# Performance work log

Hardware: AMD Instinct MI355X
Metric: run time of the kernel (lower is better)

## Reference

```python
import jax, jax.numpy as jnp
import numpy as np

B, T, NF, C, H, TOPK = 4, 8, 8192, 384, 12, 32
D = C // H
SCALE = D ** -0.5  # qk_scale=None -> head_dim**-0.5


def setup_inputs() -> dict:
    key = jax.random.key(0)
    ks = jax.random.split(key, 4)
    x = jax.random.normal(ks[0], (B, T + NF, C), jnp.float32)
    qs_w = jax.random.normal(ks[1], (T, C, C), jnp.float32) * (C ** -0.5)
    kv_w = jax.random.normal(ks[2], (C, 2 * C), jnp.float32) * (C ** -0.5)
    experts_w = jax.random.normal(ks[3], (T, C, C), jnp.float32) * (C ** -0.5)
    return {"x": x, "qs_w": qs_w, "kv_w": kv_w, "experts_w": experts_w}


def reference(x, qs_w, kv_w, experts_w):
    # x: [B, T+NF, C]; first T tokens are task tokens, rest are feature tokens
    feature = x[:, T:, :]                                          # [B,NF,C]
    kv = (feature @ kv_w).reshape(B, NF, 2, H, D)                  # out dim splits [2,H,D]
    k = kv[:, :, 0].transpose(0, 2, 1, 3)                          # [B,H,NF,D]
    v = kv[:, :, 1].transpose(0, 2, 1, 3)                          # [B,H,NF,D]
    # per-task query linears (no bias), one task token each
    q = jnp.einsum('btc,tco->bto', x[:, :T, :], qs_w)              # [B,T,C]
    q = q.reshape(B, T, H, D).transpose(0, 2, 1, 3)                # [B,H,T,D]
    attn = jnp.einsum('bhtd,bhnd->bhtn', q, k) * SCALE             # [B,H,T,NF]
    vals, idx = jax.lax.top_k(attn, TOPK)                          # [B,H,T,K]
    w = jax.nn.softmax(vals, axis=-1)                              # softmax over top-k only
    # attn_token = (scatter(topk softmax) @ v) == weighted gather of v rows
    v_g = jnp.take_along_axis(v[:, :, None], idx[..., None], axis=3)   # [B,H,T,K,D]
    attn_token = jnp.einsum('bhtk,bhtkd->bhtd', w, v_g)
    attn_token = attn_token.transpose(0, 2, 1, 3).reshape(B, T, C)     # [B,T,C]
    # gather raw feature tokens at top-k indices, weight, scatter into padded zeros
    fm = feature.reshape(B, NF, H, D).transpose(0, 2, 1, 3)        # [B,H,NF,D]
    f_g = jnp.take_along_axis(fm[:, :, None], idx[..., None], axis=3) * w[..., None]  # [B,H,T,K,D]
    bi = jnp.arange(B)[:, None, None, None]
    hi = jnp.arange(H)[None, :, None, None]
    ti = jnp.arange(T)[None, None, :, None]
    # topk indices are unique per row -> set is well-defined
    feature_pad = jnp.zeros((B, H, T, NF, D), x.dtype).at[bi, hi, ti, idx].set(f_g)
    feature_pad = feature_pad.transpose(0, 2, 3, 1, 4).reshape(B, T, NF, C)  # [B,T,NF,C]
    # per-task expert linears; einsum with ones weight == sum over tasks
    feature_out = jnp.einsum('btnc,tco->bno', feature_pad, experts_w)  # [B,NF,C]
    token_out = jnp.einsum('btc,tco->bto', attn_token, experts_w)      # [B,T,C]
    return jnp.concatenate([token_out, feature_out], axis=1)          # [B,T+NF,C]
```

## Files before the change

kernel.cpp:

```cpp
#include <hip/hip_runtime.h>
#include <hip/hip_bf16.h>
#include <math.h>

#define B 4
#define T 8
#define NF 8192
#define C 384
#define H 12
#define TOPK 32
#define D 32
#define STOT (T + NF)
#define R (H * T)
#define KSEL 48
#define NCH 4
#define CHSZ (NF / NCH)
#define SCALE 0.17677669529663687f

typedef unsigned int uint;
typedef unsigned short ushort;
typedef short bf16x8 __attribute__((ext_vector_type(8)));
typedef float f32x4 __attribute__((ext_vector_type(4)));

__device__ __forceinline__ ushort bf16u(float a) {
  return __builtin_bit_cast(ushort, __float2bfloat16(a));
}

__device__ __forceinline__ ushort f32_key(float s) {
  uint kb = bf16u(s);
  kb ^= (kb & 0x8000u) ? 0xFFFFu : 0x8000u;
  return (ushort)kb;
}

__global__ __launch_bounds__(256) void ta_qproj_kernel(
    const float* __restrict__ x, const float* __restrict__ qs_w,
    float* __restrict__ q_part) {
  int t = blockIdx.x;
  int o0 = blockIdx.y * 64;
  int z = blockIdx.z;
  int tid = threadIdx.x;
  int o = tid & 63, ks = tid >> 6;
  __shared__ float xs[B][192];
  __shared__ float part[4][B][64];
  if (tid < 192) {
    int b = tid / 48, j4 = (tid % 48) * 4;
    *reinterpret_cast<float4*>(&xs[b][j4]) =
        *reinterpret_cast<const float4*>(x + ((size_t)b * STOT + t) * C + z * 192 + j4);
  }
  __syncthreads();
  float a0 = 0.f, a1 = 0.f, a2 = 0.f, a3 = 0.f;
  const float* w = qs_w + (size_t)t * C * C + (size_t)(z * 192 + ks * 48) * C + o0 + o;
#pragma unroll 8
  for (int c = 0; c < 48; ++c) {
    float wv = w[(size_t)c * C];
    int cj = ks * 48 + c;
    a0 += xs[0][cj] * wv;
    a1 += xs[1][cj] * wv;
    a2 += xs[2][cj] * wv;
    a3 += xs[3][cj] * wv;
  }
  part[ks][0][o] = a0; part[ks][1][o] = a1;
  part[ks][2][o] = a2; part[ks][3][o] = a3;
  __syncthreads();
  {
    int b = tid >> 6, oo = tid & 63;
    float s = part[0][b][oo] + part[1][b][oo] + part[2][b][oo] + part[3][b][oo];
    q_part[(((size_t)z * B + b) * T + t) * C + o0 + oo] = s;
  }
}

__global__ __launch_bounds__(384) void ta_fold_kernel(
    const float* __restrict__ q_part, const float* __restrict__ kv_w,
    float* __restrict__ qk_f32, ushort* __restrict__ qk_bf) {
  int b = blockIdx.x / H, h = blockIdx.x % H;
  int tid = threadIdx.x;
  __shared__ float kS[C][33];
  __shared__ float qh[T][D];
  if (tid < T * D) {
    int t = tid >> 5, d = tid & 31;
    qh[t][d] = q_part[((size_t)b * T + t) * C + h * D + d] +
               q_part[(((size_t)B + b) * T + t) * C + h * D + d];
  }
  for (int j = tid; j < C * 8; j += 384) {
    int c = j >> 3, d4 = (j & 7) * 4;
    float4 v = *reinterpret_cast<const float4*>(
        kv_w + (size_t)c * (2 * C) + h * D + d4);
    kS[c][d4 + 0] = v.x; kS[c][d4 + 1] = v.y;
    kS[c][d4 + 2] = v.z; kS[c][d4 + 3] = v.w;
  }
  __syncthreads();
  float acc[T] = {0.f, 0.f, 0.f, 0.f, 0.f, 0.f, 0.f, 0.f};
#pragma unroll
  for (int d = 0; d < D; ++d) {
    float kv = kS[tid][d];
#pragma unroll
    for (int t = 0; t < T; ++t) acc[t] += qh[t][d] * kv;
  }
#pragma unroll
  for (int t = 0; t < T; ++t) {
    size_t off = ((size_t)b * R + (size_t)h * T + t) * C + tid;
    float a = acc[t];
    qk_f32[off] = a;
    qk_bf[off] = bf16u(a);
  }
}

__global__ __launch_bounds__(256) void ta_scores_kernel(
    const float* __restrict__ x, const ushort* __restrict__ qk_bf,
    ushort* __restrict__ keys, float4* __restrict__ out4) {
  int b = blockIdx.y;
  int n0 = blockIdx.x * 64;
  int tid = threadIdx.x;
  int lane = tid & 63, w = tid >> 6;
  int row16 = lane & 15, kg = lane >> 4;
  __shared__ ushort fS[64][72];
  __shared__ ushort qS[96][72];
  f32x4 acc[6];
#pragma unroll
  for (int i = 0; i < 6; ++i) acc[i] = (f32x4){0.f, 0.f, 0.f, 0.f};

  {
    const int SL = (B * STOT * C / 4) / 512;
    int zbid = blockIdx.y * gridDim.x + blockIdx.x;
    float4 z = {0.f, 0.f, 0.f, 0.f};
    float4* dst = out4 + (size_t)zbid * SL;
    for (int j = tid; j < SL; j += 256) dst[j] = z;
  }

  const float* xb = x + ((size_t)b * STOT + T + n0) * C;
  const ushort* qb = qk_bf + (size_t)b * R * C;

  int frow = tid >> 2, fcg = (tid & 3) * 8;

#pragma unroll 1
  for (int c0 = 0; c0 < C; c0 += 32) {
    {
      const float* src = xb + (size_t)frow * C + c0 + fcg;
      float4 v0 = *reinterpret_cast<const float4*>(src);
      float4 v1 = *reinterpret_cast<const float4*>(src + 4);
      uint4 p;
      p.x = (uint)bf16u(v0.x) | ((uint)bf16u(v0.y) << 16);
      p.y = (uint)bf16u(v0.z) | ((uint)bf16u(v0.w) << 16);
      p.z = (uint)bf16u(v1.x) | ((uint)bf16u(v1.y) << 16);
      p.w = (uint)bf16u(v1.z) | ((uint)bf16u(v1.w) << 16);
      *reinterpret_cast<uint4*>(&fS[frow][fcg]) = p;
    }
#pragma unroll
    for (int s = 0; s < 2; ++s) {
      int u = tid + 256 * s;
      if (u < 384) {
        int row = u >> 2, cg = (u & 3) * 8;
        uint4 v = *reinterpret_cast<const uint4*>(qb + (size_t)row * C + c0 + cg);
        *reinterpret_cast<uint4*>(&qS[row][cg]) = v;
      }
    }
    __syncthreads();
    bf16x8 bfr = *reinterpret_cast<const bf16x8*>(&fS[w * 16 + row16][kg * 8]);
#pragma unroll
    for (int i = 0; i < 6; ++i) {
      bf16x8 afr = *reinterpret_cast<const bf16x8*>(&qS[i * 16 + row16][kg * 8]);
      acc[i] = __builtin_amdgcn_mfma_f32_16x16x32_bf16(afr, bfr, acc[i], 0, 0, 0);
    }
    __syncthreads();
  }
  int n = n0 + w * 16 + row16;
#pragma unroll
  for (int i = 0; i < 6; ++i) {
    int rbase = i * 16 + kg * 4;
#pragma unroll
    for (int reg = 0; reg < 4; ++reg) {
      keys[((size_t)b * R + rbase + reg) * NF + n] = f32_key(acc[i][reg] * SCALE);
    }
  }
}

__global__ __launch_bounds__(256) void ta_selchunk_kernel(
    const ushort* __restrict__ keys, uint* __restrict__ cand_buf) {
  int ch = blockIdx.x, rr = blockIdx.y;
  int tid = threadIdx.x;
  int lane = tid & 63, wvi = tid >> 6;
  __shared__ uint hist[4096];
  __shared__ uint cand[CHSZ];
  __shared__ uint wtot[4];
  __shared__ uint sh_piv, cnt;
  const ushort* kp = keys + (size_t)rr * NF + (size_t)ch * CHSZ;

  {
    uint4 z4 = {0u, 0u, 0u, 0u};
    uint4* hz = reinterpret_cast<uint4*>(hist);
    for (int i = tid; i < 1024; i += 256) hz[i] = z4;
  }
  if (tid == 0) cnt = 0;
  __syncthreads();
  for (int i = tid; i < CHSZ; i += 256) atomicAdd(&hist[kp[i] >> 4], 1u);
  __syncthreads();

  uint pp = 0;
#pragma unroll
  for (int j = 0; j < 16; ++j) pp += hist[tid * 16 + j];
  uint suf = pp;
#pragma unroll
  for (int off = 1; off < 64; off <<= 1) {
    uint o = __shfl_down(suf, off);
    if (lane + off < 64) suf += o;
  }
  if (lane == 0) wtot[wvi] = suf;
  __syncthreads();
  {
    uint later = 0;
    for (int wq = wvi + 1; wq < 4; ++wq) later += wtot[wq];
    uint geg = later + suf;
    uint gng = geg - pp;
    if (geg >= (uint)KSEL && gng < (uint)KSEL) {
      uint run = gng;
      int pv = 0;
      for (int j = 15; j >= 0; --j) {
        uint c = hist[tid * 16 + j];
        uint nrun = run + c;
        if (nrun >= (uint)KSEL && run < (uint)KSEL) pv = tid * 16 + j;
        run = nrun;
      }
      sh_piv = (uint)pv;
    }
  }
  __syncthreads();
  uint piv = sh_piv;
  for (int i = tid; i < CHSZ; i += 256) {
    uint u = kp[i];
    if ((u >> 4) >= piv) {
      uint s = atomicAdd(&cnt, 1u);
      cand[s] = (u << 13) | (8191u - (uint)(ch * CHSZ + i));
    }
  }
  __syncthreads();
  uint m = cnt;
  for (int i2 = tid; i2 < (int)m; i2 += 256) {
    uint me = cand[i2];
    int r = 0;
    for (uint e = 0; e < m; ++e) r += (cand[e] > me);
    if (r < KSEL) cand_buf[((size_t)rr * NCH + ch) * KSEL + r] = me;
  }
}

__global__ __launch_bounds__(384) void ta_mergetail_kernel(
    const uint* __restrict__ cand_buf, const float* __restrict__ x,
    const float* __restrict__ qk_f32, const float* __restrict__ kv_w,
    const float* __restrict__ ew, float* __restrict__ out) {
  constexpr int M = NCH * KSEL;
  int rr = blockIdx.x;
  int t = rr % T, h = (rr / T) % H, b = rr / R;
  int hD = h * D;
  int tid = threadIdx.x;
  __shared__ uint candS[M];
  __shared__ int il[KSEL];
  __shared__ float sv[KSEL];
  __shared__ int rkS[KSEL];
  __shared__ float qS[C];
  __shared__ float wl[TOPK];
  __shared__ int top_il[TOPK];
  __shared__ float fbarS[C];
  __shared__ float gS[TOPK][D];
  __shared__ float part[8][D];
  __shared__ __align__(16) float attS[D];
  __shared__ float smax, esum;

  if (tid < M) candS[tid] = cand_buf[(size_t)rr * M + tid];
  qS[tid] = qk_f32[(size_t)rr * C + tid];
  __syncthreads();
  if (tid < M) {
    uint me = candS[tid];
    int r = 0;
#pragma unroll 8
    for (int e = 0; e < M; ++e) r += (candS[e] > me);
    if (r < KSEL) il[r] = 8191 - (int)(me & 8191u);
  }
  __syncthreads();

  {
    int k = tid >> 3, j = tid & 7;
    const float* fp = x + ((size_t)b * STOT + T + il[k]) * C + j;
    float s = 0.f;
#pragma unroll 8
    for (int m2 = 0; m2 < 48; ++m2) s += fp[m2 * 8] * qS[j + m2 * 8];
    s += __shfl_down(s, 4);
    s += __shfl_down(s, 2);
    s += __shfl_down(s, 1);
    if (j == 0) sv[k] = s * SCALE;
  }
  __syncthreads();
  if (tid < KSEL) {
    float mys = sv[tid];
    int myn = il[tid];
    int r = 0;
#pragma unroll
    for (int e = 0; e < KSEL; ++e) {
      float se = sv[e];
      r += (se > mys) || (se == mys && il[e] < myn);
    }
    rkS[tid] = r;
    if (r == 0) smax = mys;
  }
  __syncthreads();
  {
    float e = 0.f;
    if (tid < KSEL && rkS[tid] < TOPK) e = expf(sv[tid] - smax);
    if (tid < 64) {
      float t2 = e;
#pragma unroll
      for (int off = 32; off; off >>= 1) t2 += __shfl_down(t2, off);
      if (tid == 0) esum = t2;
    }
    __syncthreads();
    if (tid < KSEL && rkS[tid] < TOPK) {
      wl[rkS[tid]] = e / esum;
      top_il[rkS[tid]] = il[tid];
    }
  }
  __syncthreads();

  {
    float fbar = 0.f;
    bool ing = (tid >= hD) && (tid < hD + D);
#pragma unroll 4
    for (int k = 0; k < TOPK; ++k) {
      float v = x[((size_t)b * STOT + T + top_il[k]) * C + tid];
      float wv = wl[k] * v;
      fbar += wv;
      if (ing) gS[k][tid - hD] = wv;
    }
    fbarS[tid] = fbar;
  }
  __syncthreads();

  if (tid < 256) {
    int d = tid & 31, seg = tid >> 5;
    const float* vw = kv_w + C + hD + d;
    float a0 = 0.f, a1 = 0.f;
    int cb = seg * 48;
#pragma unroll 8
    for (int c = 0; c < 48; c += 2) {
      a0 += fbarS[cb + c] * vw[(size_t)(cb + c) * (2 * C)];
      a1 += fbarS[cb + c + 1] * vw[(size_t)(cb + c + 1) * (2 * C)];
    }
    part[seg][d] = a0 + a1;
  }
  __syncthreads();
  if (tid < D) {
    float a = 0.f;
#pragma unroll
    for (int s = 0; s < 8; ++s) a += part[s][tid];
    attS[tid] = a;
  }
  __syncthreads();

  float ewc[D];
  const float* ewt = ew + (size_t)t * C * C + (size_t)hD * C + tid;
#pragma unroll
  for (int dd = 0; dd < D; ++dd) ewc[dd] = ewt[(size_t)dd * C];
  size_t obase = (size_t)b * STOT * C + tid;
#pragma unroll 1
  for (int kk = 0; kk < TOPK; ++kk) {
    float y = 0.f;
#pragma unroll
    for (int d4 = 0; d4 < D; d4 += 4) {
      float4 g4 = *reinterpret_cast<const float4*>(&gS[kk][d4]);
      y += g4.x * ewc[d4] + g4.y * ewc[d4 + 1] +
           g4.z * ewc[d4 + 2] + g4.w * ewc[d4 + 3];
    }
    atomicAdd(&out[obase + (size_t)(T + top_il[kk]) * C], y);
  }
  {
    float y = 0.f;
#pragma unroll
    for (int d4 = 0; d4 < D; d4 += 4) {
      float4 a4 = *reinterpret_cast<const float4*>(attS + d4);
      y += a4.x * ewc[d4] + a4.y * ewc[d4 + 1] +
           a4.z * ewc[d4 + 2] + a4.w * ewc[d4 + 3];
    }
    atomicAdd(&out[obase + (size_t)t * C], y);
  }
}

extern "C" void kernel_launch(void* const* d_in, const int* in_sizes, int n_in,
                              void* d_out, int out_size, void* d_ws, size_t ws_size,
                              hipStream_t stream) {
  const float* x = (const float*)d_in[0];
  const float* qs_w = (const float*)d_in[1];
  const float* kv_w = (const float*)d_in[2];
  const float* ew = (const float*)d_in[3];
  float* out = (float*)d_out;

  char* p = (char*)d_ws;
  float* qk_f32 = (float*)p;  p += (size_t)B * R * C * 4;
  ushort* qk_bf = (ushort*)p; p += (size_t)B * R * C * 2;
  ushort* keys = (ushort*)p;  p += (size_t)B * R * NF * 2;
  uint* cand_buf = (uint*)p;  p += (size_t)B * R * NCH * KSEL * 4;
  float* q_part = (float*)p;

  dim3 gq(T, C / 64, 2);
  ta_qproj_kernel<<<gq, 256, 0, stream>>>(x, qs_w, q_part);
  ta_fold_kernel<<<B * H, 384, 0, stream>>>(q_part, kv_w, qk_f32, qk_bf);
  dim3 g2(NF / 64, B);
  ta_scores_kernel<<<g2, 256, 0, stream>>>(x, qk_bf, keys, (float4*)out);
  dim3 gs(NCH, B * R);
  ta_selchunk_kernel<<<gs, 256, 0, stream>>>(keys, cand_buf);
  ta_mergetail_kernel<<<B * R, 384, 0, stream>>>(cand_buf, x, qk_f32, kv_w, ew, out);
}
```

Baseline: 83.81 us.

## Use split-bf16 triple MFMA for scores and drop fp32 rescoring of candidates

The score GEMM now splits both operands into hi and lo bf16 parts and runs three MFMAs per step, giving near-fp32 scores. It writes those scores to a full fp32 buffer, so the merge kernel ranks candidates by a lookup instead of recomputing 48 dot products from x and qk_f32. Zeroing of the output moves from the scores kernel to the selection kernel. The cost is three times the MFMA work, doubled LDS staging, and an extra 1.5 MB fp32 score write.

```diff
diff --git a/kernel.cpp b/kernel.cpp
--- a/kernel.cpp
+++ b/kernel.cpp
@@ -24,7 +24,10 @@
 __device__ __forceinline__ ushort bf16u(float a) {
   return __builtin_bit_cast(ushort, __float2bfloat16(a));
 }
-
+__device__ __forceinline__ float bf16f(ushort u) {
+  uint v = (uint)u << 16;
+  return __builtin_bit_cast(float, v);
+}
 __device__ __forceinline__ ushort f32_key(float s) {
   uint kb = bf16u(s);
   kb ^= (kb & 0x8000u) ? 0xFFFFu : 0x8000u;
@@ -70,7 +73,7 @@
 
 __global__ __launch_bounds__(384) void ta_fold_kernel(
     const float* __restrict__ q_part, const float* __restrict__ kv_w,
-    float* __restrict__ qk_f32, ushort* __restrict__ qk_bf) {
+    ushort* __restrict__ qk_hi, ushort* __restrict__ qk_lo) {
   int b = blockIdx.x / H, h = blockIdx.x % H;
   int tid = threadIdx.x;
   __shared__ float kS[C][33];
@@ -99,35 +102,30 @@
   for (int t = 0; t < T; ++t) {
     size_t off = ((size_t)b * R + (size_t)h * T + t) * C + tid;
     float a = acc[t];
-    qk_f32[off] = a;
-    qk_bf[off] = bf16u(a);
+    ushort hh = bf16u(a);
+    qk_hi[off] = hh;
+    qk_lo[off] = bf16u(a - bf16f(hh));
   }
 }
 
 __global__ __launch_bounds__(256) void ta_scores_kernel(
-    const float* __restrict__ x, const ushort* __restrict__ qk_bf,
-    ushort* __restrict__ keys, float4* __restrict__ out4) {
+    const float* __restrict__ x, const ushort* __restrict__ qk_hi,
+    const ushort* __restrict__ qk_lo, ushort* __restrict__ keys,
+    float* __restrict__ scoresF) {
   int b = blockIdx.y;
   int n0 = blockIdx.x * 64;
   int tid = threadIdx.x;
   int lane = tid & 63, w = tid >> 6;
   int row16 = lane & 15, kg = lane >> 4;
-  __shared__ ushort fS[64][72];
-  __shared__ ushort qS[96][72];
+  __shared__ ushort fH[64][72], fL[64][72];
+  __shared__ ushort qH[96][72], qL[96][72];
   f32x4 acc[6];
 #pragma unroll
   for (int i = 0; i < 6; ++i) acc[i] = (f32x4){0.f, 0.f, 0.f, 0.f};
 
-  {
-    const int SL = (B * STOT * C / 4) / 512;
-    int zbid = blockIdx.y * gridDim.x + blockIdx.x;
-    float4 z = {0.f, 0.f, 0.f, 0.f};
-    float4* dst = out4 + (size_t)zbid * SL;
-    for (int j = tid; j < SL; j += 256) dst[j] = z;
-  }
-
   const float* xb = x + ((size_t)b * STOT + T + n0) * C;
-  const ushort* qb = qk_bf + (size_t)b * R * C;
+  const ushort* qhb = qk_hi + (size_t)b * R * C;
+  const ushort* qlb = qk_lo + (size_t)b * R * C;
 
   int frow = tid >> 2, fcg = (tid & 3) * 8;
 
@@ -137,28 +135,48 @@
       const float* src = xb + (size_t)frow * C + c0 + fcg;
       float4 v0 = *reinterpret_cast<const float4*>(src);
       float4 v1 = *reinterpret_cast<const float4*>(src + 4);
-      uint4 p;
-      p.x = (uint)bf16u(v0.x) | ((uint)bf16u(v0.y) << 16);
-      p.y = (uint)bf16u(v0.z) | ((uint)bf16u(v0.w) << 16);
-      p.z = (uint)bf16u(v1.x) | ((uint)bf16u(v1.y) << 16);
-      p.w = (uint)bf16u(v1.z) | ((uint)bf16u(v1.w) << 16);
-      *reinterpret_cast<uint4*>(&fS[frow][fcg]) = p;
-    }
-#pragma unroll
-    for (int s = 0; s < 2; ++s) {
+      float vv[8] = {v0.x, v0.y, v0.z, v0.w, v1.x, v1.y, v1.z, v1.w};
+      ushort hh[8], ll[8];
+#pragma unroll
+      for (int j = 0; j < 8; ++j) {
+        hh[j] = bf16u(vv[j]);
+        ll[j] = bf16u(vv[j] - bf16f(hh[j]));
+      }
+      uint4 ph, pl;
+      ph.x = (uint)hh[0] | ((uint)hh[1] << 16);
+      ph.y = (uint)hh[2] | ((uint)hh[3] << 16);
+      ph.z = (uint)hh[4] | ((uint)hh[5] << 16);
+      ph.w = (uint)hh[6] | ((uint)hh[7] << 16);
+      pl.x = (uint)ll[0] | ((uint)ll[1] << 16);
+      pl.y = (uint)ll[2] | ((uint)ll[3] << 16);
+      pl.z = (uint)ll[4] | ((uint)ll[5] << 16);
+      pl.w = (uint)ll[6] | ((uint)ll[7] << 16);
+      *reinterpret_cast<uint4*>(&fH[frow][fcg]) = ph;
+      *reinterpret_cast<uint4*>(&fL[frow][fcg]) = pl;
+    }
+#pragma unroll
+    for (int s = 0; s < 3; ++s) {
       int u = tid + 256 * s;
+      int v = (u >= 384) ? u - 384 : u;
+      int row = v >> 2, cg = (v & 3) * 8;
       if (u < 384) {
-        int row = u >> 2, cg = (u & 3) * 8;
-        uint4 v = *reinterpret_cast<const uint4*>(qb + (size_t)row * C + c0 + cg);
-        *reinterpret_cast<uint4*>(&qS[row][cg]) = v;
+        uint4 t4 = *reinterpret_cast<const uint4*>(qhb + (size_t)row * C + c0 + cg);
+        *reinterpret_cast<uint4*>(&qH[row][cg]) = t4;
+      } else {
+        uint4 t4 = *reinterpret_cast<const uint4*>(qlb + (size_t)row * C + c0 + cg);
+        *reinterpret_cast<uint4*>(&qL[row][cg]) = t4;
       }
     }
     __syncthreads();
-    bf16x8 bfr = *reinterpret_cast<const bf16x8*>(&fS[w * 16 + row16][kg * 8]);
+    bf16x8 bh = *reinterpret_cast<const bf16x8*>(&fH[w * 16 + row16][kg * 8]);
+    bf16x8 bl = *reinterpret_cast<const bf16x8*>(&fL[w * 16 + row16][kg * 8]);
 #pragma unroll
     for (int i = 0; i < 6; ++i) {
-      bf16x8 afr = *reinterpret_cast<const bf16x8*>(&qS[i * 16 + row16][kg * 8]);
-      acc[i] = __builtin_amdgcn_mfma_f32_16x16x32_bf16(afr, bfr, acc[i], 0, 0, 0);
+      bf16x8 ah = *reinterpret_cast<const bf16x8*>(&qH[i * 16 + row16][kg * 8]);
+      bf16x8 al = *reinterpret_cast<const bf16x8*>(&qL[i * 16 + row16][kg * 8]);
+      acc[i] = __builtin_amdgcn_mfma_f32_16x16x32_bf16(ah, bh, acc[i], 0, 0, 0);
+      acc[i] = __builtin_amdgcn_mfma_f32_16x16x32_bf16(ah, bl, acc[i], 0, 0, 0);
+      acc[i] = __builtin_amdgcn_mfma_f32_16x16x32_bf16(al, bh, acc[i], 0, 0, 0);
     }
     __syncthreads();
   }
@@ -168,13 +186,17 @@
     int rbase = i * 16 + kg * 4;
 #pragma unroll
     for (int reg = 0; reg < 4; ++reg) {
-      keys[((size_t)b * R + rbase + reg) * NF + n] = f32_key(acc[i][reg] * SCALE);
+      float s = acc[i][reg] * SCALE;
+      size_t off = ((size_t)b * R + rbase + reg) * NF + n;
+      keys[off] = f32_key(s);
+      scoresF[off] = s;
     }
   }
 }
 
 __global__ __launch_bounds__(256) void ta_selchunk_kernel(
-    const ushort* __restrict__ keys, uint* __restrict__ cand_buf) {
+    const ushort* __restrict__ keys, uint* __restrict__ cand_buf,
+    float4* __restrict__ out4) {
   int ch = blockIdx.x, rr = blockIdx.y;
   int tid = threadIdx.x;
   int lane = tid & 63, wvi = tid >> 6;
@@ -183,6 +205,12 @@
   __shared__ uint wtot[4];
   __shared__ uint sh_piv, cnt;
   const ushort* kp = keys + (size_t)rr * NF + (size_t)ch * CHSZ;
+
+  {
+    float4 z = {0.f, 0.f, 0.f, 0.f};
+    float4* dst = out4 + (size_t)(rr * NCH + ch) * 2050;
+    for (int j = tid; j < 2050; j += 256) dst[j] = z;
+  }
 
   {
     uint4 z4 = {0u, 0u, 0u, 0u};
@@ -242,19 +270,16 @@
 }
 
 __global__ __launch_bounds__(384) void ta_mergetail_kernel(
-    const uint* __restrict__ cand_buf, const float* __restrict__ x,
-    const float* __restrict__ qk_f32, const float* __restrict__ kv_w,
+    const uint* __restrict__ cand_buf, const float* __restrict__ scoresF,
+    const float* __restrict__ x, const float* __restrict__ kv_w,
     const float* __restrict__ ew, float* __restrict__ out) {
   constexpr int M = NCH * KSEL;
   int rr = blockIdx.x;
   int t = rr % T, h = (rr / T) % H, b = rr / R;
   int hD = h * D;
   int tid = threadIdx.x;
-  __shared__ uint candS[M];
-  __shared__ int il[KSEL];
-  __shared__ float sv[KSEL];
-  __shared__ int rkS[KSEL];
-  __shared__ float qS[C];
+  __shared__ float sfS[M];
+  __shared__ int idxS[M];
   __shared__ float wl[TOPK];
   __shared__ int top_il[TOPK];
   __shared__ float fbarS[C];
@@ -263,46 +288,29 @@
   __shared__ __align__(16) float attS[D];
   __shared__ float smax, esum;
 
-  if (tid < M) candS[tid] = cand_buf[(size_t)rr * M + tid];
-  qS[tid] = qk_f32[(size_t)rr * C + tid];
-  __syncthreads();
   if (tid < M) {
-    uint me = candS[tid];
+    uint me = cand_buf[(size_t)rr * M + tid];
+    int idx = 8191 - (int)(me & 8191u);
+    idxS[tid] = idx;
+    sfS[tid] = scoresF[(size_t)rr * NF + idx];
+  }
+  __syncthreads();
+  if (tid < M) {
+    float mys = sfS[tid];
+    int myn = idxS[tid];
     int r = 0;
 #pragma unroll 8
-    for (int e = 0; e < M; ++e) r += (candS[e] > me);
-    if (r < KSEL) il[r] = 8191 - (int)(me & 8191u);
-  }
-  __syncthreads();
-
-  {
-    int k = tid >> 3, j = tid & 7;
-    const float* fp = x + ((size_t)b * STOT + T + il[k]) * C + j;
-    float s = 0.f;
-#pragma unroll 8
-    for (int m2 = 0; m2 < 48; ++m2) s += fp[m2 * 8] * qS[j + m2 * 8];
-    s += __shfl_down(s, 4);
-    s += __shfl_down(s, 2);
-    s += __shfl_down(s, 1);
-    if (j == 0) sv[k] = s * SCALE;
-  }
-  __syncthreads();
-  if (tid < KSEL) {
-    float mys = sv[tid];
-    int myn = il[tid];
-    int r = 0;
-#pragma unroll
-    for (int e = 0; e < KSEL; ++e) {
-      float se = sv[e];
-      r += (se > mys) || (se == mys && il[e] < myn);
-    }
-    rkS[tid] = r;
+    for (int e = 0; e < M; ++e) {
+      float se = sfS[e];
+      r += (se > mys) || (se == mys && idxS[e] < myn);
+    }
+    if (r < TOPK) { wl[r] = mys; top_il[r] = myn; }
     if (r == 0) smax = mys;
   }
   __syncthreads();
   {
     float e = 0.f;
-    if (tid < KSEL && rkS[tid] < TOPK) e = expf(sv[tid] - smax);
+    if (tid < TOPK) e = expf(wl[tid] - smax);
     if (tid < 64) {
       float t2 = e;
 #pragma unroll
@@ -310,10 +318,7 @@
       if (tid == 0) esum = t2;
     }
     __syncthreads();
-    if (tid < KSEL && rkS[tid] < TOPK) {
-      wl[rkS[tid]] = e / esum;
-      top_il[rkS[tid]] = il[tid];
-    }
+    if (tid < TOPK) wl[tid] = e / esum;
   }
   __syncthreads();
 
@@ -390,18 +395,19 @@
   float* out = (float*)d_out;
 
   char* p = (char*)d_ws;
-  float* qk_f32 = (float*)p;  p += (size_t)B * R * C * 4;
-  ushort* qk_bf = (ushort*)p; p += (size_t)B * R * C * 2;
-  ushort* keys = (ushort*)p;  p += (size_t)B * R * NF * 2;
-  uint* cand_buf = (uint*)p;  p += (size_t)B * R * NCH * KSEL * 4;
+  ushort* qk_hi = (ushort*)p;  p += (size_t)B * R * C * 2;
+  ushort* qk_lo = (ushort*)p;  p += (size_t)B * R * C * 2;
+  ushort* keys = (ushort*)p;   p += (size_t)B * R * NF * 2;
+  float* scoresF = (float*)p;  p += (size_t)B * R * NF * 4;
+  uint* cand_buf = (uint*)p;   p += (size_t)B * R * NCH * KSEL * 4;
   float* q_part = (float*)p;
 
   dim3 gq(T, C / 64, 2);
   ta_qproj_kernel<<<gq, 256, 0, stream>>>(x, qs_w, q_part);
-  ta_fold_kernel<<<B * H, 384, 0, stream>>>(q_part, kv_w, qk_f32, qk_bf);
+  ta_fold_kernel<<<B * H, 384, 0, stream>>>(q_part, kv_w, qk_hi, qk_lo);
   dim3 g2(NF / 64, B);
-  ta_scores_kernel<<<g2, 256, 0, stream>>>(x, qk_bf, keys, (float4*)out);
+  ta_scores_kernel<<<g2, 256, 0, stream>>>(x, qk_hi, qk_lo, keys, scoresF);
   dim3 gs(NCH, B * R);
-  ta_selchunk_kernel<<<gs, 256, 0, stream>>>(keys, cand_buf);
-  ta_mergetail_kernel<<<B * R, 384, 0, stream>>>(cand_buf, x, qk_f32, kv_w, ew, out);
-}
+  ta_selchunk_kernel<<<gs, 256, 0, stream>>>(keys, cand_buf, (float4*)out);
+  ta_mergetail_kernel<<<B * R, 384, 0, stream>>>(cand_buf, scoresF, x, kv_w, ew, out);
+}
```

Result: slower. 88.63 us (+5.7%).

## Split merge and tail into separate kernels and quarter top-k across blocks

Applied to the files above, without the earlier changes.

The fused merge+tail kernel becomes two kernels. A merge kernel writes the softmax weights and top-k indices to a workspace buffer. A tail kernel then launches four blocks per (b,h,t) row, each handling 8 of the 32 selected tokens and their partial contributions to the token output. Because the value projection and expert product are linear, the partial results can be combined with the existing atomic adds. This raises the block count of the tail stage fourfold to improve occupancy and latency hiding. The cost is one extra launch, a workspace round trip, reloading the expert-weight columns four times per row, and more atomics on the token outputs.

```diff
diff --git a/kernel.cpp b/kernel.cpp
--- a/kernel.cpp
+++ b/kernel.cpp
@@ -24,7 +24,6 @@
 __device__ __forceinline__ ushort bf16u(float a) {
   return __builtin_bit_cast(ushort, __float2bfloat16(a));
 }
-
 __device__ __forceinline__ ushort f32_key(float s) {
   uint kb = bf16u(s);
   kb ^= (kb & 0x8000u) ? 0xFFFFu : 0x8000u;
@@ -241,26 +240,19 @@
   }
 }
 
-__global__ __launch_bounds__(384) void ta_mergetail_kernel(
+__global__ __launch_bounds__(384) void ta_merge_kernel(
     const uint* __restrict__ cand_buf, const float* __restrict__ x,
-    const float* __restrict__ qk_f32, const float* __restrict__ kv_w,
-    const float* __restrict__ ew, float* __restrict__ out) {
+    const float* __restrict__ qk_f32, float* __restrict__ w_buf,
+    int* __restrict__ idx_buf) {
   constexpr int M = NCH * KSEL;
   int rr = blockIdx.x;
-  int t = rr % T, h = (rr / T) % H, b = rr / R;
-  int hD = h * D;
+  int b = rr / R;
   int tid = threadIdx.x;
   __shared__ uint candS[M];
   __shared__ int il[KSEL];
   __shared__ float sv[KSEL];
   __shared__ int rkS[KSEL];
   __shared__ float qS[C];
-  __shared__ float wl[TOPK];
-  __shared__ int top_il[TOPK];
-  __shared__ float fbarS[C];
-  __shared__ float gS[TOPK][D];
-  __shared__ float part[8][D];
-  __shared__ __align__(16) float attS[D];
   __shared__ float smax, esum;
 
   if (tid < M) candS[tid] = cand_buf[(size_t)rr * M + tid];
@@ -300,29 +292,49 @@
     if (r == 0) smax = mys;
   }
   __syncthreads();
-  {
-    float e = 0.f;
-    if (tid < KSEL && rkS[tid] < TOPK) e = expf(sv[tid] - smax);
-    if (tid < 64) {
-      float t2 = e;
-#pragma unroll
-      for (int off = 32; off; off >>= 1) t2 += __shfl_down(t2, off);
-      if (tid == 0) esum = t2;
-    }
-    __syncthreads();
-    if (tid < KSEL && rkS[tid] < TOPK) {
-      wl[rkS[tid]] = e / esum;
-      top_il[rkS[tid]] = il[tid];
-    }
+  float e = 0.f;
+  if (tid < KSEL && rkS[tid] < TOPK) e = expf(sv[tid] - smax);
+  if (tid < 64) {
+    float t2 = e;
+#pragma unroll
+    for (int off = 32; off; off >>= 1) t2 += __shfl_down(t2, off);
+    if (tid == 0) esum = t2;
+  }
+  __syncthreads();
+  if (tid < KSEL && rkS[tid] < TOPK) {
+    w_buf[(size_t)rr * TOPK + rkS[tid]] = e / esum;
+    idx_buf[(size_t)rr * TOPK + rkS[tid]] = il[tid];
+  }
+}
+
+__global__ __launch_bounds__(384) void ta_tail_kernel(
+    const float* __restrict__ x, const float* __restrict__ kv_w,
+    const float* __restrict__ ew, const float* __restrict__ w_buf,
+    const int* __restrict__ idx_buf, float* __restrict__ out) {
+  constexpr int KQ = TOPK / 4;
+  int q = blockIdx.x & 3, rr = blockIdx.x >> 2;
+  int t = rr % T, h = (rr / T) % H, b = rr / R;
+  int hD = h * D;
+  int tid = threadIdx.x;
+  __shared__ float wl[KQ];
+  __shared__ int il[KQ];
+  __shared__ float fbarS[C];
+  __shared__ float gS[KQ][D];
+  __shared__ float part[8][D];
+  __shared__ __align__(16) float attS[D];
+
+  if (tid < KQ) {
+    wl[tid] = w_buf[(size_t)rr * TOPK + q * KQ + tid];
+    il[tid] = idx_buf[(size_t)rr * TOPK + q * KQ + tid];
   }
   __syncthreads();
 
   {
     float fbar = 0.f;
     bool ing = (tid >= hD) && (tid < hD + D);
-#pragma unroll 4
-    for (int k = 0; k < TOPK; ++k) {
-      float v = x[((size_t)b * STOT + T + top_il[k]) * C + tid];
+#pragma unroll
+    for (int k = 0; k < KQ; ++k) {
+      float v = x[((size_t)b * STOT + T + il[k]) * C + tid];
       float wv = wl[k] * v;
       fbar += wv;
       if (ing) gS[k][tid - hD] = wv;
@@ -358,7 +370,7 @@
   for (int dd = 0; dd < D; ++dd) ewc[dd] = ewt[(size_t)dd * C];
   size_t obase = (size_t)b * STOT * C + tid;
 #pragma unroll 1
-  for (int kk = 0; kk < TOPK; ++kk) {
+  for (int kk = 0; kk < KQ; ++kk) {
     float y = 0.f;
 #pragma unroll
     for (int d4 = 0; d4 < D; d4 += 4) {
@@ -366,7 +378,7 @@
       y += g4.x * ewc[d4] + g4.y * ewc[d4 + 1] +
            g4.z * ewc[d4 + 2] + g4.w * ewc[d4 + 3];
     }
-    atomicAdd(&out[obase + (size_t)(T + top_il[kk]) * C], y);
+    atomicAdd(&out[obase + (size_t)(T + il[kk]) * C], y);
   }
   {
     float y = 0.f;
@@ -394,6 +406,8 @@
   ushort* qk_bf = (ushort*)p; p += (size_t)B * R * C * 2;
   ushort* keys = (ushort*)p;  p += (size_t)B * R * NF * 2;
   uint* cand_buf = (uint*)p;  p += (size_t)B * R * NCH * KSEL * 4;
+  float* w_buf = (float*)p;   p += (size_t)B * R * TOPK * 4;
+  int* idx_buf = (int*)p;     p += (size_t)B * R * TOPK * 4;
   float* q_part = (float*)p;
 
   dim3 gq(T, C / 64, 2);
@@ -403,5 +417,6 @@
   ta_scores_kernel<<<g2, 256, 0, stream>>>(x, qk_bf, keys, (float4*)out);
   dim3 gs(NCH, B * R);
   ta_selchunk_kernel<<<gs, 256, 0, stream>>>(keys, cand_buf);
-  ta_mergetail_kernel<<<B * R, 384, 0, stream>>>(cand_buf, x, qk_f32, kv_w, ew, out);
-}
+  ta_merge_kernel<<<B * R, 384, 0, stream>>>(cand_buf, x, qk_f32, w_buf, idx_buf);
+  ta_tail_kernel<<<4 * B * R, 384, 0, stream>>>(x, kv_w, ew, w_buf, idx_buf, out);
+}
```

New measurement: 84.54 us. Within noise of the previous version (+0.9%).
